# Kernel optimization log

Hardware: AMD Instinct MI355X
Metric: run time of the kernel (lower is better)

The kernel has to match this reference:

```python
import jax, jax.numpy as jnp
import numpy as np

B, N, C, K = 8, 4096, 256, 8192

def setup_inputs() -> dict:
    key = jax.random.key(0)
    k1, k2 = jax.random.split(key)
    z_e_x = jax.random.normal(k1, (B, N, C), dtype=jnp.float32)
    # codebook initialized like the torch module: normal(0,1) rescaled so mean row norm = sqrt(D)
    cb = jax.random.normal(k2, (K, C), dtype=jnp.float32)
    cur = jnp.mean(jnp.linalg.norm(cb, axis=1))
    cb = cb * (jnp.sqrt(jnp.float32(C)) / cur)
    return {"z_e_x": z_e_x, "codebook": cb}

def reference(z_e_x, codebook):
    """VQ straight-through forward: returns (codes, idx, distances).
    codes: [B,N,C] nearest codebook vectors; idx: [B,N] int32 indices;
    distances: [B,N] min squared L2 distances."""
    b, n, c = z_e_x.shape
    x = z_e_x.astype(jnp.float32).reshape(b * n, c)          # [BN, C]
    cb = codebook.astype(jnp.float32)                        # [K, C]
    cb_sq = jnp.sum(cb * cb, axis=1)                         # [K]
    x_sq = jnp.sum(x * x, axis=1, keepdims=True)             # [BN,1]
    l2 = x_sq + cb_sq[None, :] - 2.0 * (x @ cb.T)            # [BN, K]
    idx_flat = jnp.argmin(l2, axis=1)                        # [BN]
    min_vals = jnp.min(l2, axis=1)                           # [BN]
    codes = jnp.take(cb, idx_flat, axis=0).reshape(b, n, c).astype(z_e_x.dtype)
    idx = idx_flat.reshape(b, n)
    distances = min_vals.reshape(b, n).astype(z_e_x.dtype)
    return codes, idx, distances
```

## Files before the change

kernel.cpp:

```cpp
#include <hip/hip_runtime.h>
#include <hip/hip_bf16.h>
#include <stdint.h>


#define M_ROWS 32768
#define KCODES 8192
#define CDIM   256
#define BM 128
#define BNT 256
#define BK 32
#define NSPLIT 2
#define KCHUNK 4096
#define NTILES 16
#define KSTEPS 8
#define NREC 32
#define MARGIN 0.75f

typedef _Float16 f16x8 __attribute__((ext_vector_type(8)));
typedef _Float16 f16x4 __attribute__((ext_vector_type(4)));
typedef float    f32x4 __attribute__((ext_vector_type(4)));

__device__ __forceinline__ unsigned umin2(unsigned a, unsigned b) { return a < b ? a : b; }
__device__ __forceinline__ unsigned umax2(unsigned a, unsigned b) { return a > b ? a : b; }

__global__ void vq_prep(const float* __restrict__ x, const float* __restrict__ cb,
                        _Float16* __restrict__ xhi, _Float16* __restrict__ cbhi,
                        float* __restrict__ xsq, float* __restrict__ cbsq) {
  const int wave = threadIdx.x >> 6, lane = threadIdx.x & 63;
  const int row = blockIdx.x * 4 + wave;
  const float* src;
  _Float16* dhi;
  float* dsq;
  if (row < M_ROWS) {
    src = x + (size_t)row * CDIM;  dhi = xhi + (size_t)row * CDIM;  dsq = xsq + row;
  } else {
    const int r = row - M_ROWS;
    src = cb + (size_t)r * CDIM;   dhi = cbhi + (size_t)r * CDIM;   dsq = cbsq + r;
  }
  const float4 v = *(const float4*)(src + lane * 4);
  f16x4 h;
  h[0] = (_Float16)(v.x * 64.0f); h[1] = (_Float16)(v.y * 64.0f);
  h[2] = (_Float16)(v.z * 64.0f); h[3] = (_Float16)(v.w * 64.0f);
  *(f16x4*)(dhi + lane * 4) = h;
  float s = v.x * v.x + v.y * v.y + v.z * v.z + v.w * v.w;
  #pragma unroll
  for (int off = 32; off > 0; off >>= 1) s += __shfl_down(s, off, 64);
  if (lane == 0) *dsq = s;
}

__device__ __forceinline__ void gl16(const _Float16* g, _Float16* l) {
  __builtin_amdgcn_global_load_lds(
      (const __attribute__((address_space(1))) unsigned int*)g,
      (__attribute__((address_space(3))) unsigned int*)l, 16, 0, 0);
}

__global__ __launch_bounds__(256, 2) void vq_pass1(
    const _Float16* __restrict__ xhi, const _Float16* __restrict__ cbhi,
    const float* __restrict__ cbsq, uint2* __restrict__ srec) {
  extern __shared__ char smem[];
  _Float16* sA = (_Float16*)smem;
  _Float16* sB = (_Float16*)(smem + BM * CDIM * 2);

  const int tid  = threadIdx.x;
  const int wave = tid >> 6, lane = tid & 63;
  const int quad = lane >> 4, l15 = lane & 15;
  const int mbase  = blockIdx.x * BM;
  const int cbase0 = blockIdx.y * KCHUNK;
  const int wrow = (wave >> 1) * 64;
  const int wcol = (wave & 1) * 128;

  {
    const int ar = lane >> 5;
    const int as = lane & 31;
    #pragma unroll
    for (int t = 0; t < 16; ++t) {
      const int rb  = (wave * 16 + t) * 2;
      const int row = rb + ar;
      const int slot = as ^ (row & 7);
      gl16(xhi + (size_t)(mbase + row) * CDIM + slot * 8, sA + rb * CDIM);
    }
  }

  const int srl  = lane >> 2;
  const int scol = (((lane & 3) ^ ((lane >> 3) & 3)) << 3);
  const int fcol = ((quad ^ ((l15 >> 1) & 3)) << 3);
  const int asw  = l15 & 7;

  unsigned k1[4][4], k2[4][4];

  for (int nt = 0; nt < NTILES; ++nt) {
    const int cb0 = cbase0 + nt * BNT;
    if ((nt & 1) == 0) {
      #pragma unroll
      for (int mf = 0; mf < 4; ++mf)
        #pragma unroll
        for (int i = 0; i < 4; ++i) { k1[mf][i] = 0x7fffffffu; k2[mf][i] = 0x7fffffffu; }
    }

    f32x4 acc[4][8];
    #pragma unroll
    for (int mf = 0; mf < 4; ++mf)
      #pragma unroll
      for (int nf = 0; nf < 8; ++nf) {
        f32x4 z = {0.0f, 0.0f, 0.0f, 0.0f};
        acc[mf][nf] = z;
      }

    for (int ks = 0; ks < KSTEPS; ++ks) {
      const int kofs = ks * BK;
      __syncthreads();
      #pragma unroll
      for (int t = 0; t < 4; ++t) {
        const int rb = wave * 64 + t * 16;
        gl16(cbhi + (size_t)(cb0 + rb + srl) * CDIM + kofs + scol, sB + rb * BK);
      }
      __syncthreads();

      f16x8 ah[4];
      #pragma unroll
      for (int mf = 0; mf < 4; ++mf) {
        const int arow = wrow + mf * 16 + l15;
        const int aslot = (ks * 4 + quad) ^ asw;
        ah[mf] = *(const f16x8*)(sA + arow * CDIM + aslot * 8);
      }
      #pragma unroll
      for (int nf = 0; nf < 8; ++nf) {
        const f16x8 bh = *(const f16x8*)(sB + (wcol + nf * 16 + l15) * BK + fcol);
        #pragma unroll
        for (int mf = 0; mf < 4; ++mf)
          acc[mf][nf] = __builtin_amdgcn_mfma_f32_16x16x32_f16(ah[mf], bh, acc[mf][nf], 0, 0, 0);
      }
    }

    #pragma unroll
    for (int nf = 0; nf < 8; ++nf) {
      const int col = cb0 + wcol + nf * 16 + l15;
      const float cq16 = fmaf(cbsq[col], 16.0f, 32768.0f);
      #pragma unroll
      for (int mf = 0; mf < 4; ++mf)
        #pragma unroll
        for (int i = 0; i < 4; ++i) {
          const float kf = fmaf(acc[mf][nf][i], -0.0078125f, cq16);
          const unsigned key = ((unsigned)kf << 13) | (unsigned)col;
          k2[mf][i] = umin2(k2[mf][i], umax2(k1[mf][i], key));
          k1[mf][i] = umin2(k1[mf][i], key);
        }
    }

    if (nt & 1) {
      const int g = blockIdx.y * 16 + (nt >> 1) * 2 + (wave & 1);
      #pragma unroll
      for (int mf = 0; mf < 4; ++mf)
        #pragma unroll
        for (int i = 0; i < 4; ++i) {
          unsigned a1 = k1[mf][i], a2 = k2[mf][i];
          #pragma unroll
          for (int m = 1; m <= 8; m <<= 1) {
            const unsigned o1 = (unsigned)__shfl_xor((int)a1, m, 64);
            const unsigned o2 = (unsigned)__shfl_xor((int)a2, m, 64);
            a2 = umin2(umin2(a2, o2), umax2(a1, o1));
            a1 = umin2(a1, o1);
          }
          if (l15 == 0) {
            const int rl = wrow + mf * 16 + quad * 4 + i;
            uint2 r; r.x = a1; r.y = a2;
            srec[(size_t)(mbase + rl) * NREC + g] = r;
          }
        }
    }
  }
}

__global__ void vq_finalize(const float* __restrict__ x, const float* __restrict__ cb,
                            const float* __restrict__ xsq, const float* __restrict__ cbsq,
                            const uint2* __restrict__ srec,
                            float* __restrict__ outIdx, float* __restrict__ outDist,
                            float* __restrict__ codes) {
  const int wave = threadIdx.x >> 6, lane = threadIdx.x & 63;
  const int row = blockIdx.x * 4 + wave;
  uint2 rec;
  if (lane < NREC) rec = srec[(size_t)row * NREC + lane];
  else { rec.x = 0x7fffffffu; rec.y = 0x7fffffffu; }
  const float v1 = (float)(rec.x >> 13) * 0.0625f - 2048.0f;
  const float v2 = (float)(rec.y >> 13) * 0.0625f - 2048.0f;
  const int c1 = (int)(rec.x & 8191u);
  const int c2 = (int)(rec.y & 8191u);

  float gm = v1;
  #pragma unroll
  for (int m = 1; m <= 32; m <<= 1) gm = fminf(gm, __shfl_xor(gm, m, 64));
  const float thr = gm + MARGIN;
  unsigned long long mask1 = __ballot(v1 <= thr);
  unsigned long long mask2 = __ballot(v2 <= thr);

  const float4 xv = *(const float4*)(x + (size_t)row * CDIM + lane * 4);
  const float xq = xsq[row];
  float best = __builtin_inff(); int bidx = 1 << 30;

  #pragma unroll
  for (int pass = 0; pass < 2; ++pass) {
    unsigned long long m = pass ? mask2 : mask1;
    const int fi = pass ? c2 : c1;
    while (m) {
      const int g = __builtin_ctzll((long long)m); m &= m - 1;
      const int ci = __shfl(fi, g, 64);
      const float4 cv = *(const float4*)(cb + (size_t)ci * CDIM + lane * 4);
      float s = xv.x * cv.x + xv.y * cv.y + xv.z * cv.z + xv.w * cv.w;
      #pragma unroll
      for (int mm = 1; mm <= 32; mm <<= 1) s += __shfl_xor(s, mm, 64);
      const float dist = xq + cbsq[ci] - 2.0f * s;
      if (dist < best || (dist == best && ci < bidx)) { best = dist; bidx = ci; }
    }
  }

  if (lane == 0) { outIdx[row] = (float)bidx; outDist[row] = best; }
  const float4 cw = *(const float4*)(cb + (size_t)bidx * CDIM + lane * 4);
  *(float4*)(codes + (size_t)row * CDIM + lane * 4) = cw;
}

extern "C" void kernel_launch(void* const* d_in, const int* in_sizes, int n_in,
                              void* d_out, int out_size, void* d_ws, size_t ws_size,
                              hipStream_t stream) {
  const float* x  = (const float*)d_in[0];
  const float* cb = (const float*)d_in[1];
  float* out = (float*)d_out;

  char* w = (char*)d_ws;
  _Float16* xhi  = (_Float16*)(w);
  _Float16* cbhi = (_Float16*)(w + 16777216);
  float*    xsq  = (float*)   (w + 20971520);
  float*    cbsq = (float*)   (w + 21102592);
  uint2*    srec = (uint2*)   (w + 21135360);

  vq_prep<<<(M_ROWS + KCODES) / 4, 256, 0, stream>>>(x, cb, xhi, cbhi, xsq, cbsq);
  const size_t smem = (size_t)BM * CDIM * 2 + (size_t)BNT * BK * 2;
  vq_pass1<<<dim3(M_ROWS / BM, NSPLIT), 256, smem, stream>>>(xhi, cbhi, cbsq, srec);
  vq_finalize<<<M_ROWS / 4, 256, 0, stream>>>(x, cb, xsq, cbsq, srec,
                                              out + 8388608, out + 8421376, out);
}
```

Measured before the change: 291.0 us.

## Pipeline codebook loads with 4-stage LDS ring and 8-wave blocks

Replaces the per-k-step double-synchronised codebook load with a 4-deep LDS ring buffer. Loads are issued two steps ahead using explicit vmcnt waits and a single barrier per step. Blocks become 512 threads over the full codebook (no K split), with each wave covering 64 columns. The codebook squared norms are staged in LDS, and MFMA sections are wrapped in setprio. The aim is to hide global-to-LDS latency and remove a barrier per step, at the cost of much larger LDS use (about 130KB) and half as many blocks, which can reduce occupancy and parallelism.

Result: faster. 283.4 us (-2.6%).

```diff
diff --git a/kernel.cpp b/kernel.cpp
--- a/kernel.cpp
+++ b/kernel.cpp
@@ -9,16 +9,15 @@
 #define BM 128
 #define BNT 256
 #define BK 32
-#define NSPLIT 2
-#define KCHUNK 4096
-#define NTILES 16
-#define KSTEPS 8
+#define NTILES 32
 #define NREC 32
 #define MARGIN 0.75f
 
 typedef _Float16 f16x8 __attribute__((ext_vector_type(8)));
 typedef _Float16 f16x4 __attribute__((ext_vector_type(4)));
 typedef float    f32x4 __attribute__((ext_vector_type(4)));
+
+#define WAITV(N) asm volatile("s_waitcnt vmcnt(" #N ")" ::: "memory")
 
 __device__ __forceinline__ unsigned umin2(unsigned a, unsigned b) { return a < b ? a : b; }
 __device__ __forceinline__ unsigned umax2(unsigned a, unsigned b) { return a > b ? a : b; }
@@ -48,36 +47,36 @@
   if (lane == 0) *dsq = s;
 }
 
-__device__ __forceinline__ void gl16(const _Float16* g, _Float16* l) {
+__device__ __forceinline__ void gl16p(const void* g, void* l) {
   __builtin_amdgcn_global_load_lds(
       (const __attribute__((address_space(1))) unsigned int*)g,
       (__attribute__((address_space(3))) unsigned int*)l, 16, 0, 0);
 }
 
-__global__ __launch_bounds__(256, 2) void vq_pass1(
+__global__ __launch_bounds__(512, 2) void vq_pass1(
     const _Float16* __restrict__ xhi, const _Float16* __restrict__ cbhi,
-    const float* __restrict__ cbsq, uint2* __restrict__ srec) {
+    const float* __restrict__ cbsqg, uint2* __restrict__ srec) {
   extern __shared__ char smem[];
-  _Float16* sA = (_Float16*)smem;
-  _Float16* sB = (_Float16*)(smem + BM * CDIM * 2);
+  _Float16* sA  = (_Float16*)smem;
+  _Float16* sB  = (_Float16*)(smem + 65536);
+  float*    sCq = (float*)(smem + 65536 + 65536);
 
   const int tid  = threadIdx.x;
   const int wave = tid >> 6, lane = tid & 63;
   const int quad = lane >> 4, l15 = lane & 15;
-  const int mbase  = blockIdx.x * BM;
-  const int cbase0 = blockIdx.y * KCHUNK;
-  const int wrow = (wave >> 1) * 64;
-  const int wcol = (wave & 1) * 128;
+  const int mbase = blockIdx.x * BM;
+  const int wrow = (wave >> 2) * 64;
+  const int wcol = (wave & 3) * 64;
 
   {
     const int ar = lane >> 5;
     const int as = lane & 31;
     #pragma unroll
-    for (int t = 0; t < 16; ++t) {
-      const int rb  = (wave * 16 + t) * 2;
+    for (int t = 0; t < 8; ++t) {
+      const int rb  = (wave * 8 + t) * 2;
       const int row = rb + ar;
       const int slot = as ^ (row & 7);
-      gl16(xhi + (size_t)(mbase + row) * CDIM + slot * 8, sA + rb * CDIM);
+      gl16p(xhi + (size_t)(mbase + row) * CDIM + slot * 8, sA + rb * CDIM);
     }
   }
 
@@ -86,36 +85,58 @@
   const int fcol = ((quad ^ ((l15 >> 1) & 3)) << 3);
   const int asw  = l15 & 7;
 
+  auto stageB = [&](int nts, int kss, int bufidx) {
+    const int cb0 = nts * BNT, kofs = kss * BK;
+    _Float16* dst = sB + bufidx * (BNT * BK);
+    #pragma unroll
+    for (int t = 0; t < 2; ++t) {
+      const int rb = wave * 32 + t * 16;
+      gl16p(cbhi + (size_t)(cb0 + rb + srl) * CDIM + kofs + scol, dst + rb * BK);
+    }
+  };
+  auto stageCq = [&](int nts) {
+    gl16p(cbsqg + nts * BNT + lane * 4, sCq + (nts & 1) * BNT);
+  };
+
+  stageB(0, 0, 0); stageCq(0);
+  stageB(0, 1, 1);
+
   unsigned k1[4][4], k2[4][4];
 
   for (int nt = 0; nt < NTILES; ++nt) {
-    const int cb0 = cbase0 + nt * BNT;
-    if ((nt & 1) == 0) {
+    const bool lastnt = (nt == NTILES - 1);
+    if ((nt & 3) == 0) {
       #pragma unroll
       for (int mf = 0; mf < 4; ++mf)
         #pragma unroll
         for (int i = 0; i < 4; ++i) { k1[mf][i] = 0x7fffffffu; k2[mf][i] = 0x7fffffffu; }
     }
 
-    f32x4 acc[4][8];
+    f32x4 acc[4][4];
     #pragma unroll
     for (int mf = 0; mf < 4; ++mf)
       #pragma unroll
-      for (int nf = 0; nf < 8; ++nf) {
+      for (int nf = 0; nf < 4; ++nf) {
         f32x4 z = {0.0f, 0.0f, 0.0f, 0.0f};
         acc[mf][nf] = z;
       }
 
-    for (int ks = 0; ks < KSTEPS; ++ks) {
-      const int kofs = ks * BK;
-      __syncthreads();
-      #pragma unroll
-      for (int t = 0; t < 4; ++t) {
-        const int rb = wave * 64 + t * 16;
-        gl16(cbhi + (size_t)(cb0 + rb + srl) * CDIM + kofs + scol, sB + rb * BK);
-      }
-      __syncthreads();
-
+    #pragma unroll
+    for (int ks = 0; ks < 8; ++ks) {
+      if (ks <= 5) {
+        stageB(nt, ks + 2, (ks + 2) & 3);
+      } else if (ks == 6) {
+        if (!lastnt) { stageB(nt + 1, 0, 0); stageCq(nt + 1); }
+      } else {
+        if (!lastnt) stageB(nt + 1, 1, 1);
+      }
+      if (ks <= 5)      WAITV(4);
+      else if (ks == 6) { if (!lastnt) WAITV(5); else WAITV(2); }
+      else              { if (!lastnt) WAITV(5); else WAITV(0); }
+      __builtin_amdgcn_s_barrier();
+      asm volatile("" ::: "memory");
+
+      const _Float16* sBc = sB + (ks & 3) * (BNT * BK);
       f16x8 ah[4];
       #pragma unroll
       for (int mf = 0; mf < 4; ++mf) {
@@ -123,19 +144,22 @@
         const int aslot = (ks * 4 + quad) ^ asw;
         ah[mf] = *(const f16x8*)(sA + arow * CDIM + aslot * 8);
       }
-      #pragma unroll
-      for (int nf = 0; nf < 8; ++nf) {
-        const f16x8 bh = *(const f16x8*)(sB + (wcol + nf * 16 + l15) * BK + fcol);
+      __builtin_amdgcn_s_setprio(1);
+      #pragma unroll
+      for (int nf = 0; nf < 4; ++nf) {
+        const f16x8 bh = *(const f16x8*)(sBc + (wcol + nf * 16 + l15) * BK + fcol);
         #pragma unroll
         for (int mf = 0; mf < 4; ++mf)
           acc[mf][nf] = __builtin_amdgcn_mfma_f32_16x16x32_f16(ah[mf], bh, acc[mf][nf], 0, 0, 0);
       }
-    }
-
-    #pragma unroll
-    for (int nf = 0; nf < 8; ++nf) {
-      const int col = cb0 + wcol + nf * 16 + l15;
-      const float cq16 = fmaf(cbsq[col], 16.0f, 32768.0f);
+      __builtin_amdgcn_s_setprio(0);
+    }
+
+    #pragma unroll
+    for (int nf = 0; nf < 4; ++nf) {
+      const int cwl = wcol + nf * 16 + l15;
+      const int col = nt * BNT + cwl;
+      const float cq16 = fmaf(sCq[(nt & 1) * BNT + cwl], 16.0f, 32768.0f);
       #pragma unroll
       for (int mf = 0; mf < 4; ++mf)
         #pragma unroll
@@ -147,8 +171,8 @@
         }
     }
 
-    if (nt & 1) {
-      const int g = blockIdx.y * 16 + (nt >> 1) * 2 + (wave & 1);
+    if ((nt & 3) == 3) {
+      const int g = (nt >> 2) * 4 + (wave & 3);
       #pragma unroll
       for (int mf = 0; mf < 4; ++mf)
         #pragma unroll
@@ -233,8 +257,8 @@
   uint2*    srec = (uint2*)   (w + 21135360);
 
   vq_prep<<<(M_ROWS + KCODES) / 4, 256, 0, stream>>>(x, cb, xhi, cbhi, xsq, cbsq);
-  const size_t smem = (size_t)BM * CDIM * 2 + (size_t)BNT * BK * 2;
-  vq_pass1<<<dim3(M_ROWS / BM, NSPLIT), 256, smem, stream>>>(xhi, cbhi, cbsq, srec);
+  const size_t smem = 65536 + 65536 + 2048;
+  vq_pass1<<<dim3(M_ROWS / BM), 512, smem, stream>>>(xhi, cbhi, cbsq, srec);
   vq_finalize<<<M_ROWS / 4, 256, 0, stream>>>(x, cb, xsq, cbsq, srec,
                                               out + 8388608, out + 8421376, out);
 }
```
